# Kernel optimization log

Measured on AMD Instinct MI355X. Metric: run time of the kernel, lower is better.

## Reference

```python
import jax, jax.numpy as jnp
import numpy as np

N_BINS = 15

def setup_inputs() -> dict:
    key = jax.random.key(0)
    k1, k2 = jax.random.split(key)
    N, C = 1048576, 128
    logits = jax.random.normal(k1, (N, C), dtype=jnp.float32)
    labels = jax.random.randint(k2, (N,), 0, C, dtype=jnp.int64)
    return {"logits": logits, "labels": labels}

def reference(logits, labels):
    # softmax + argmax: confidences = max prob, predictions = argmax
    probs = jax.nn.softmax(logits, axis=1)
    conf = jnp.max(probs, axis=1)                      # [N]
    pred = jnp.argmax(probs, axis=1)                   # [N]
    acc = (pred == labels).astype(conf.dtype)          # [N]
    # bin i covers (i/n_bins, (i+1)/n_bins]; conf > 1/C > 0 so ceil-1 lands in-range
    bins = jnp.clip(jnp.ceil(conf * N_BINS).astype(jnp.int32) - 1, 0, N_BINS - 1)
    ones = jnp.ones_like(conf)
    counts = jax.ops.segment_sum(ones, bins, num_segments=N_BINS)
    conf_sum = jax.ops.segment_sum(conf, bins, num_segments=N_BINS)
    acc_sum = jax.ops.segment_sum(acc, bins, num_segments=N_BINS)
    n = jnp.asarray(conf.shape[0], conf.dtype)
    safe = jnp.maximum(counts, 1.0)
    per_bin = jnp.abs(conf_sum / safe - acc_sum / safe) * (counts / n)
    ece = jnp.sum(jnp.where(counts > 0, per_bin, 0.0))
    return ece.reshape(1)
```

## Files before the change

kernel.cpp:

```cpp
#include <hip/hip_runtime.h>

#define N_BINS 15
#define GRID_MAIN 2048
#define BLOCK 256
#define ROWS_PER_GRP 4

typedef float f32x4 __attribute__((ext_vector_type(4)));

__global__ __launch_bounds__(BLOCK) void ece_main(const float* __restrict__ logits,
                                                  const int* __restrict__ labels,
                                                  float* __restrict__ partial,
                                                  int N, int nBlocks) {
    __shared__ float s_acc[3 * N_BINS];
    const int tid = threadIdx.x;
    if (tid < 3 * N_BINS) s_acc[tid] = 0.f;
    __syncthreads();

    const int grp = tid >> 4;
    const int sub = tid & 15;

    auto process = [&](const f32x4 a, const f32x4 b, int lab, int row) {
        const int i0 = sub * 4, i1 = 64 + sub * 4;
        float m = a[0]; int mi = i0;
        if (a[1] > m) { m = a[1]; mi = i0 + 1; }
        if (a[2] > m) { m = a[2]; mi = i0 + 2; }
        if (a[3] > m) { m = a[3]; mi = i0 + 3; }
        if (b[0] > m) { m = b[0]; mi = i1; }
        if (b[1] > m) { m = b[1]; mi = i1 + 1; }
        if (b[2] > m) { m = b[2]; mi = i1 + 2; }
        if (b[3] > m) { m = b[3]; mi = i1 + 3; }
        #pragma unroll
        for (int off = 8; off > 0; off >>= 1) {
            float om = __shfl_xor(m, off);
            int   oi = __shfl_xor(mi, off);
            if (om > m || (om == m && oi < mi)) { m = om; mi = oi; }
        }
        float s = __expf(a[0] - m) + __expf(a[1] - m) + __expf(a[2] - m) + __expf(a[3] - m)
                + __expf(b[0] - m) + __expf(b[1] - m) + __expf(b[2] - m) + __expf(b[3] - m);
        #pragma unroll
        for (int off = 8; off > 0; off >>= 1)
            s += __shfl_xor(s, off);
        if (sub == 0) {
            const float conf = 1.0f / s;
            int bin = (int)ceilf(conf * (float)N_BINS) - 1;
            bin = min(max(bin, 0), N_BINS - 1);
            const float acc = (mi == lab) ? 1.0f : 0.0f;
            atomicAdd(&s_acc[bin],              1.0f);
            atomicAdd(&s_acc[N_BINS + bin],     conf);
            atomicAdd(&s_acc[2 * N_BINS + bin], acc);
        }
    };

    const int rowsPerIter = (BLOCK >> 4) * ROWS_PER_GRP;
    const int rowStride   = nBlocks * rowsPerIter;

    for (int tile = blockIdx.x * rowsPerIter; tile < N; tile += rowStride) {
        const int base = tile + grp * ROWS_PER_GRP;
        if (tile + rowsPerIter <= N) {
            f32x4 va[ROWS_PER_GRP], vb[ROWS_PER_GRP];
            int   lab[ROWS_PER_GRP];
            #pragma unroll
            for (int j = 0; j < ROWS_PER_GRP; ++j) {
                const f32x4* rp = (const f32x4*)(logits + (size_t)(base + j) * 128);
                va[j]  = __builtin_nontemporal_load(rp + sub);
                vb[j]  = __builtin_nontemporal_load(rp + 16 + sub);
                lab[j] = labels[base + j];
            }
            #pragma unroll
            for (int j = 0; j < ROWS_PER_GRP; ++j)
                process(va[j], vb[j], lab[j], base + j);
        } else {
            #pragma unroll
            for (int j = 0; j < ROWS_PER_GRP; ++j) {
                if (base + j < N) {
                    const f32x4* rp = (const f32x4*)(logits + (size_t)(base + j) * 128);
                    process(rp[sub], rp[16 + sub], labels[base + j], base + j);
                }
            }
        }
    }

    __syncthreads();
    if (tid < 3 * N_BINS)
        partial[(size_t)tid * nBlocks + blockIdx.x] = s_acc[tid];
}

__global__ __launch_bounds__(1024) void ece_final(const float* __restrict__ partial,
                                                  float* __restrict__ out,
                                                  int nBlocks, float invN) {
    __shared__ float red[3 * N_BINS];
    const int tid = threadIdx.x;
    const int w = tid >> 6, lane = tid & 63;
    for (int s = w; s < 3 * N_BINS; s += 16) {
        float sum = 0.f;
        for (int i = lane; i < nBlocks; i += 64)
            sum += partial[(size_t)s * nBlocks + i];
        #pragma unroll
        for (int off = 32; off > 0; off >>= 1)
            sum += __shfl_xor(sum, off);
        if (lane == 0) red[s] = sum;
    }
    __syncthreads();
    if (tid == 0) {
        float ece = 0.f;
        #pragma unroll
        for (int b = 0; b < N_BINS; ++b) {
            if (red[b] > 0.f)
                ece += fabsf(red[N_BINS + b] - red[2 * N_BINS + b]) * invN;
        }
        out[0] = ece;
    }
}

extern "C" void kernel_launch(void* const* d_in, const int* in_sizes, int n_in,
                              void* d_out, int out_size, void* d_ws, size_t ws_size,
                              hipStream_t stream) {
    const float* logits = (const float*)d_in[0];
    const int*   labels = (const int*)d_in[1];
    float*       out    = (float*)d_out;
    float*       partial = (float*)d_ws;

    const int N = in_sizes[1];

    int grid = GRID_MAIN;
    const int rowsPerIter = (BLOCK >> 4) * ROWS_PER_GRP;
    if ((size_t)grid * rowsPerIter > (size_t)N)
        grid = (N + rowsPerIter - 1) / rowsPerIter;

    ece_main<<<grid, BLOCK, 0, stream>>>(logits, labels, partial, N, grid);
    ece_final<<<1, 1024, 0, stream>>>(partial, out, grid, 1.0f / (float)N);
}
```

Before: 682.6 us.

## Double-buffer logits tiles in registers to overlap loads with compute

Restructures the grid-stride loop into a software pipeline: the next tile's logits and labels are loaded into a second register tile while the current tile is reduced. This is meant to hide global memory latency within each wave. It also adds a min-blocks-per-SM hint to launch_bounds to limit register use. The doubled register footprint may cost occupancy or cause spills, and the tail handling moves to a single block.

```diff
diff --git a/kernel.cpp b/kernel.cpp
--- a/kernel.cpp
+++ b/kernel.cpp
@@ -3,14 +3,32 @@
 #define N_BINS 15
 #define GRID_MAIN 2048
 #define BLOCK 256
-#define ROWS_PER_GRP 4
+#define ROWS 4
 
 typedef float f32x4 __attribute__((ext_vector_type(4)));
 
-__global__ __launch_bounds__(BLOCK) void ece_main(const float* __restrict__ logits,
-                                                  const int* __restrict__ labels,
-                                                  float* __restrict__ partial,
-                                                  int N, int nBlocks) {
+
+struct Tile {
+    f32x4 a[ROWS];
+    f32x4 b[ROWS];
+    int   lab[ROWS];
+};
+
+__device__ __forceinline__ void stage(Tile& t, const float* __restrict__ logits,
+                                      const int* __restrict__ labels, int base, int sub) {
+    #pragma unroll
+    for (int j = 0; j < ROWS; ++j) {
+        const f32x4* rp = (const f32x4*)(logits + (size_t)(base + j) * 128);
+        t.a[j]   = __builtin_nontemporal_load(rp + sub);
+        t.b[j]   = __builtin_nontemporal_load(rp + 16 + sub);
+        t.lab[j] = labels[base + j];
+    }
+}
+
+__global__ __launch_bounds__(BLOCK, 4) void ece_main(const float* __restrict__ logits,
+                                                     const int* __restrict__ labels,
+                                                     float* __restrict__ partial,
+                                                     int N, int nBlocks) {
     __shared__ float s_acc[3 * N_BINS];
     const int tid = threadIdx.x;
     if (tid < 3 * N_BINS) s_acc[tid] = 0.f;
@@ -19,7 +37,7 @@
     const int grp = tid >> 4;
     const int sub = tid & 15;
 
-    auto process = [&](const f32x4 a, const f32x4 b, int lab, int row) {
+    auto processRow = [&](const f32x4 a, const f32x4 b, int lab) {
         const int i0 = sub * 4, i1 = 64 + sub * 4;
         float m = a[0]; int mi = i0;
         if (a[1] > m) { m = a[1]; mi = i0 + 1; }
@@ -51,31 +69,39 @@
         }
     };
 
-    const int rowsPerIter = (BLOCK >> 4) * ROWS_PER_GRP;
-    const int rowStride   = nBlocks * rowsPerIter;
+    auto computeTile = [&](const Tile& t) {
+        #pragma unroll
+        for (int j = 0; j < ROWS; ++j)
+            processRow(t.a[j], t.b[j], t.lab[j]);
+    };
 
-    for (int tile = blockIdx.x * rowsPerIter; tile < N; tile += rowStride) {
-        const int base = tile + grp * ROWS_PER_GRP;
-        if (tile + rowsPerIter <= N) {
-            f32x4 va[ROWS_PER_GRP], vb[ROWS_PER_GRP];
-            int   lab[ROWS_PER_GRP];
-            #pragma unroll
-            for (int j = 0; j < ROWS_PER_GRP; ++j) {
+    const int rowsPerTile = (BLOCK >> 4) * ROWS;
+    const int nFullTiles  = N / rowsPerTile;
+    const int grpOff      = grp * ROWS;
+
+    int t = blockIdx.x;
+    if (t < nFullTiles) {
+        Tile A, B;
+        stage(A, logits, labels, t * rowsPerTile + grpOff, sub);
+        int tn = t + nBlocks;
+        bool aLive = true;
+        while (tn < nFullTiles) {
+            if (aLive) { stage(B, logits, labels, tn * rowsPerTile + grpOff, sub); computeTile(A); }
+            else       { stage(A, logits, labels, tn * rowsPerTile + grpOff, sub); computeTile(B); }
+            aLive = !aLive;
+            tn += nBlocks;
+        }
+        if (aLive) computeTile(A); else computeTile(B);
+    }
+
+    const int tailStart = nFullTiles * rowsPerTile;
+    if (tailStart < N && blockIdx.x == (nFullTiles % nBlocks)) {
+        const int base = tailStart + grpOff;
+        #pragma unroll
+        for (int j = 0; j < ROWS; ++j) {
+            if (base + j < N) {
                 const f32x4* rp = (const f32x4*)(logits + (size_t)(base + j) * 128);
-                va[j]  = __builtin_nontemporal_load(rp + sub);
-                vb[j]  = __builtin_nontemporal_load(rp + 16 + sub);
-                lab[j] = labels[base + j];
-            }
-            #pragma unroll
-            for (int j = 0; j < ROWS_PER_GRP; ++j)
-                process(va[j], vb[j], lab[j], base + j);
-        } else {
-            #pragma unroll
-            for (int j = 0; j < ROWS_PER_GRP; ++j) {
-                if (base + j < N) {
-                    const f32x4* rp = (const f32x4*)(logits + (size_t)(base + j) * 128);
-                    process(rp[sub], rp[16 + sub], labels[base + j], base + j);
-                }
+                processRow(rp[sub], rp[16 + sub], labels[base + j]);
             }
         }
     }
@@ -123,9 +149,9 @@
     const int N = in_sizes[1];
 
     int grid = GRID_MAIN;
-    const int rowsPerIter = (BLOCK >> 4) * ROWS_PER_GRP;
-    if ((size_t)grid * rowsPerIter > (size_t)N)
-        grid = (N + rowsPerIter - 1) / rowsPerIter;
+    const int rowsPerTile = (BLOCK >> 4) * ROWS;
+    if ((size_t)grid * rowsPerTile > (size_t)N)
+        grid = (N + rowsPerTile - 1) / rowsPerTile;
 
     ece_main<<<grid, BLOCK, 0, stream>>>(logits, labels, partial, N, grid);
     ece_final<<<1, 1024, 0, stream>>>(partial, out, grid, 1.0f / (float)N);
```

After: 710.0 us. 1.04x slower.
